# Kernel optimization log

Hardware: AMD Instinct MI355X
Metric: run time of the kernel (lower is better)

## Reference

```python
import jax, jax.numpy as jnp
import numpy as np

K = 24  # number of clusters (all ids in [0,K) assumed present per image)
DELTA_VAR = 1.0
DELTA_DIST = 2.0
VAR_W = 1.0
DIST_W = 1.0
REG_W = 1.0


def setup_inputs() -> dict:
    key = jax.random.key(0)
    k1, k2 = jax.random.split(key)
    data = jax.random.normal(k1, (4, 16, 512, 1024), dtype=jnp.float32)
    labels = jax.random.randint(k2, (4, 512, 1024), 0, K, dtype=jnp.int32)
    return {"data": data, "labels": labels}


def reference(data, labels):
    B, D, H, Wd = data.shape
    N = H * Wd
    # [B, N, D] points, [B*N] global segment ids (batch-offset cluster ids)
    X = jnp.transpose(data.reshape(B, D, N), (0, 2, 1)).reshape(B * N, D)
    seg = (labels.reshape(B, N) + jnp.arange(B, dtype=labels.dtype)[:, None] * K).reshape(-1)

    # per-cluster sums and counts -> centers  [B*K, D]
    sums = jax.ops.segment_sum(X, seg, num_segments=B * K)
    counts = jax.ops.segment_sum(jnp.ones((B * N,), X.dtype), seg, num_segments=B * K)
    centers_flat = sums / counts[:, None]
    centers = centers_flat.reshape(B, K, D)
    counts_bk = counts.reshape(B, K)

    # variance term: per-point hinged distance to own cluster center
    c_per_point = centers_flat[seg]                      # [B*N, D]
    pt_dist = jnp.linalg.norm(X - c_per_point, axis=1)   # [B*N]
    hv = jnp.maximum(pt_dist - DELTA_VAR, 0.0) ** 2
    var_per_cluster = jax.ops.segment_sum(hv, seg, num_segments=B * K).reshape(B, K) / counts_bk
    var_sum = var_per_cluster.sum()

    # distance term: pairwise center distances (diagonal kept, as in original,
    # contributing a constant delta_dist**2 per cluster)
    diff = centers[:, :, None, :] - centers[:, None, :, :]     # [B, K, K, D]
    sq = jnp.sum(diff * diff, axis=-1)                         # [B, K, K]
    eye = jnp.eye(K, dtype=bool)[None]
    cdist = jnp.where(eye, 0.0, jnp.sqrt(jnp.where(eye, 1.0, sq)))
    hd = jnp.maximum(DELTA_DIST - cdist, 0.0) ** 2
    dist_sum = hd.sum() / (2.0 * K * (K - 1))

    # regularization: mean center norm per image, summed over batch
    reg_sum = jnp.linalg.norm(centers, axis=2).mean(axis=1).sum()

    loss = (VAR_W * var_sum + DIST_W * dist_sum + REG_W * reg_sum) / B
    return loss
```

## Files before the change

### kernel.cpp

```cpp
#include <hip/hip_runtime.h>
#include <math.h>

#define KC 24
constexpr int D = 16;
constexpr int B = 4;
constexpr int N = 512 * 1024;
constexpr float DELTA_VAR = 1.0f;
constexpr float DELTA_DIST = 2.0f;

constexpr int REP = 8;
constexpr int RS  = KC * 17;
constexpr int CS  = 33;
constexpr int PTS = 1024;
constexpr int BLOCKS = (B * N) / PTS;


__global__ __launch_bounds__(256) void k_sums(const float* __restrict__ data,
                                              const int* __restrict__ labels,
                                              float* __restrict__ g_sums,
                                              float* __restrict__ g_cnt) {
    __shared__ float s_sum[REP * RS];
    __shared__ float s_cnt[REP * CS];
    const int t = threadIdx.x;
    for (int i = t; i < REP * RS; i += 256) s_sum[i] = 0.f;
    for (int i = t; i < REP * CS; i += 256) s_cnt[i] = 0.f;
    __syncthreads();

    const int chunk = blockIdx.x * PTS;
    const int b     = chunk >> 19;
    const int n0    = (chunk & (N - 1)) + t * 4;

    const int4 lab = *(const int4*)(labels + chunk + t * 4);
    const int rbase = (t & 7) * RS;
    const int ax = rbase + lab.x * 17;
    const int ay = rbase + lab.y * 17;
    const int az = rbase + lab.z * 17;
    const int aw = rbase + lab.w * 17;

    const float* base = data + (size_t)(b * D) * N + n0;
    float4 cur = *(const float4*)(base);
#pragma unroll
    for (int d = 0; d < D; ++d) {
        float4 nxt;
        if (d < D - 1) nxt = *(const float4*)(base + (size_t)(d + 1) * N);
        atomicAdd(&s_sum[ax + d], cur.x);
        atomicAdd(&s_sum[ay + d], cur.y);
        atomicAdd(&s_sum[az + d], cur.z);
        atomicAdd(&s_sum[aw + d], cur.w);
        cur = nxt;
    }
    const int cbase = (t & 7) * CS;
    atomicAdd(&s_cnt[cbase + lab.x], 1.f);
    atomicAdd(&s_cnt[cbase + lab.y], 1.f);
    atomicAdd(&s_cnt[cbase + lab.z], 1.f);
    atomicAdd(&s_cnt[cbase + lab.w], 1.f);
    __syncthreads();

    const int rot = (blockIdx.x * 131) & 255;
    for (int i = t; i < KC * D; i += 256) {
        int j = (i + rot) % (KC * D);
        int c = j >> 4, d = j & 15;
        float s = 0.f;
#pragma unroll
        for (int r = 0; r < REP; ++r) s += s_sum[r * RS + c * 17 + d];
        atomicAdd(&g_sums[b * (KC * D) + j], s);
    }
    if (t < KC) {
        float s = 0.f;
#pragma unroll
        for (int r = 0; r < REP; ++r) s += s_cnt[r * CS + t];
        atomicAdd(&g_cnt[b * KC + t], s);
    }
}

__global__ __launch_bounds__(256) void k_var(const float* __restrict__ data,
                                             const int* __restrict__ labels,
                                             const float* __restrict__ g_sums,
                                             const float* __restrict__ g_cnt,
                                             float* __restrict__ g_varp) {
    __shared__ float s_c[KC * 17];
    __shared__ float s_ic[KC];
    __shared__ float s_part[4];
    const int t = threadIdx.x;
    const int chunk = blockIdx.x * PTS;
    const int b     = chunk >> 19;
    const int n0    = (chunk & (N - 1)) + t * 4;

    for (int i = t; i < KC * D; i += 256) {
        int c = i >> 4, d = i & 15;
        s_c[c * 17 + d] = g_sums[b * (KC * D) + i] / g_cnt[b * KC + c];
    }
    if (t < KC) s_ic[t] = 1.f / g_cnt[b * KC + t];
    __syncthreads();

    const int4 lab = *(const int4*)(labels + chunk + t * 4);
    const int ax = lab.x * 17, ay = lab.y * 17, az = lab.z * 17, aw = lab.w * 17;

    const float* base = data + (size_t)(b * D) * N + n0;
    float4 acc = {0.f, 0.f, 0.f, 0.f};
    float4 cur = *(const float4*)(base);
#pragma unroll
    for (int d = 0; d < D; ++d) {
        float4 nxt;
        if (d < D - 1) nxt = *(const float4*)(base + (size_t)(d + 1) * N);
        float df;
        df = cur.x - s_c[ax + d]; acc.x += df * df;
        df = cur.y - s_c[ay + d]; acc.y += df * df;
        df = cur.z - s_c[az + d]; acc.z += df * df;
        df = cur.w - s_c[aw + d]; acc.w += df * df;
        cur = nxt;
    }
    float h, hsum;
    h = fmaxf(sqrtf(acc.x) - DELTA_VAR, 0.f); hsum  = h * h * s_ic[lab.x];
    h = fmaxf(sqrtf(acc.y) - DELTA_VAR, 0.f); hsum += h * h * s_ic[lab.y];
    h = fmaxf(sqrtf(acc.z) - DELTA_VAR, 0.f); hsum += h * h * s_ic[lab.z];
    h = fmaxf(sqrtf(acc.w) - DELTA_VAR, 0.f); hsum += h * h * s_ic[lab.w];

    for (int o = 32; o > 0; o >>= 1) hsum += __shfl_down(hsum, o, 64);
    if ((t & 63) == 0) s_part[t >> 6] = hsum;
    __syncthreads();
    if (t == 0)
        atomicAdd(&g_varp[blockIdx.x & 63],
                  s_part[0] + s_part[1] + s_part[2] + s_part[3]);
}

__global__ __launch_bounds__(128) void k_final(const float* __restrict__ g_sums,
                                               const float* __restrict__ g_cnt,
                                               const float* __restrict__ g_varp,
                                               float* __restrict__ out) {
    __shared__ float s_c[B * KC * 17];
    __shared__ float s_red[2];
    const int t = threadIdx.x;

    float acc = 0.f;
    if (t < B * KC) {
        float cnt = g_cnt[t];
        float ns = 0.f;
        for (int d = 0; d < D; ++d) {
            float c = g_sums[t * D + d] / cnt;
            s_c[t * 17 + d] = c;
            ns += c * c;
        }
        acc = sqrtf(ns) / (float)KC;
    }
    if (t < 64) acc += g_varp[t];
    __syncthreads();

    float dacc = 0.f;
    for (int idx = t; idx < B * KC * KC; idx += 128) {
        int b = idx / (KC * KC);
        int r = idx % (KC * KC);
        int i = r / KC, j = r % KC;
        float hd;
        if (i == j) {
            hd = DELTA_DIST * DELTA_DIST;
        } else {
            const float* ci = &s_c[(b * KC + i) * 17];
            const float* cj = &s_c[(b * KC + j) * 17];
            float sq = 0.f;
            for (int d = 0; d < D; ++d) { float df = ci[d] - cj[d]; sq += df * df; }
            float hh = fmaxf(DELTA_DIST - sqrtf(sq), 0.f);
            hd = hh * hh;
        }
        dacc += hd;
    }
    float total = acc + dacc / (2.f * KC * (KC - 1));

    for (int o = 32; o > 0; o >>= 1) total += __shfl_down(total, o, 64);
    if ((t & 63) == 0) s_red[t >> 6] = total;
    __syncthreads();
    if (t == 0) out[0] = (s_red[0] + s_red[1]) / (float)B;
}

extern "C" void kernel_launch(void* const* d_in, const int* in_sizes, int n_in,
                              void* d_out, int out_size, void* d_ws, size_t ws_size,
                              hipStream_t stream) {
    const float* data  = (const float*)d_in[0];
    const int* labels  = (const int*)d_in[1];
    float* ws = (float*)d_ws;
    float* g_sums = ws;
    float* g_cnt  = ws + B * KC * D;
    float* g_varp = g_cnt + B * KC;

    hipMemsetAsync(d_ws, 0, (B * KC * D + B * KC + 64) * sizeof(float), stream);

    k_sums<<<BLOCKS, 256, 0, stream>>>(data, labels, g_sums, g_cnt);
    k_var <<<BLOCKS, 256, 0, stream>>>(data, labels, g_sums, g_cnt, g_varp);
    k_final<<<1, 128, 0, stream>>>(g_sums, g_cnt, g_varp, (float*)d_out);
}
```

Baseline: 357.5 us.

## Slice global accumulators by block and batch all point loads upfront

Global sums and counts are split into 8 slices chosen by block index, so fewer blocks contend on the same global atomic addresses. Consumers (k_var, k_final) reduce the slices when building centers. Both kernels now issue all 16 float4 loads up front instead of a one-ahead prefetch, which exposes more memory-level parallelism. This costs extra registers and slightly more work per k_var block to reduce the slices.

```diff
diff --git a/kernel.cpp b/kernel.cpp
--- a/kernel.cpp
+++ b/kernel.cpp
@@ -13,6 +13,7 @@
 constexpr int CS  = 33;
 constexpr int PTS = 1024;
 constexpr int BLOCKS = (B * N) / PTS;
+constexpr int SL = 8;
 
 
 __global__ __launch_bounds__(256) void k_sums(const float* __restrict__ data,
@@ -38,24 +39,28 @@
     const int aw = rbase + lab.w * 17;
 
     const float* base = data + (size_t)(b * D) * N + n0;
-    float4 cur = *(const float4*)(base);
-#pragma unroll
-    for (int d = 0; d < D; ++d) {
-        float4 nxt;
-        if (d < D - 1) nxt = *(const float4*)(base + (size_t)(d + 1) * N);
-        atomicAdd(&s_sum[ax + d], cur.x);
-        atomicAdd(&s_sum[ay + d], cur.y);
-        atomicAdd(&s_sum[az + d], cur.z);
-        atomicAdd(&s_sum[aw + d], cur.w);
-        cur = nxt;
-    }
+    float4 v[D];
+#pragma unroll
+    for (int d = 0; d < D; ++d) v[d] = *(const float4*)(base + (size_t)d * N);
+
     const int cbase = (t & 7) * CS;
     atomicAdd(&s_cnt[cbase + lab.x], 1.f);
     atomicAdd(&s_cnt[cbase + lab.y], 1.f);
     atomicAdd(&s_cnt[cbase + lab.z], 1.f);
     atomicAdd(&s_cnt[cbase + lab.w], 1.f);
-    __syncthreads();
-
+
+#pragma unroll
+    for (int d = 0; d < D; ++d) {
+        atomicAdd(&s_sum[ax + d], v[d].x);
+        atomicAdd(&s_sum[ay + d], v[d].y);
+        atomicAdd(&s_sum[az + d], v[d].z);
+        atomicAdd(&s_sum[aw + d], v[d].w);
+    }
+    __syncthreads();
+
+    const int slice = blockIdx.x & (SL - 1);
+    float* gs = g_sums + slice * (B * KC * D) + b * (KC * D);
+    float* gc = g_cnt  + slice * (B * KC)     + b * KC;
     const int rot = (blockIdx.x * 131) & 255;
     for (int i = t; i < KC * D; i += 256) {
         int j = (i + rot) % (KC * D);
@@ -63,13 +68,13 @@
         float s = 0.f;
 #pragma unroll
         for (int r = 0; r < REP; ++r) s += s_sum[r * RS + c * 17 + d];
-        atomicAdd(&g_sums[b * (KC * D) + j], s);
+        atomicAdd(&gs[j], s);
     }
     if (t < KC) {
         float s = 0.f;
 #pragma unroll
         for (int r = 0; r < REP; ++r) s += s_cnt[r * CS + t];
-        atomicAdd(&g_cnt[b * KC + t], s);
+        atomicAdd(&gc[t], s);
     }
 }
 
@@ -86,29 +91,38 @@
     const int b     = chunk >> 19;
     const int n0    = (chunk & (N - 1)) + t * 4;
 
+    if (t < KC) {
+        float cn = 0.f;
+#pragma unroll
+        for (int r = 0; r < SL; ++r) cn += g_cnt[r * (B * KC) + b * KC + t];
+        s_ic[t] = 1.f / cn;
+    }
+    __syncthreads();
     for (int i = t; i < KC * D; i += 256) {
         int c = i >> 4, d = i & 15;
-        s_c[c * 17 + d] = g_sums[b * (KC * D) + i] / g_cnt[b * KC + c];
-    }
-    if (t < KC) s_ic[t] = 1.f / g_cnt[b * KC + t];
+        float s = 0.f;
+#pragma unroll
+        for (int r = 0; r < SL; ++r) s += g_sums[r * (B * KC * D) + b * (KC * D) + i];
+        s_c[c * 17 + d] = s * s_ic[c];
+    }
     __syncthreads();
 
     const int4 lab = *(const int4*)(labels + chunk + t * 4);
     const int ax = lab.x * 17, ay = lab.y * 17, az = lab.z * 17, aw = lab.w * 17;
 
     const float* base = data + (size_t)(b * D) * N + n0;
+    float4 v[D];
+#pragma unroll
+    for (int d = 0; d < D; ++d) v[d] = *(const float4*)(base + (size_t)d * N);
+
     float4 acc = {0.f, 0.f, 0.f, 0.f};
-    float4 cur = *(const float4*)(base);
 #pragma unroll
     for (int d = 0; d < D; ++d) {
-        float4 nxt;
-        if (d < D - 1) nxt = *(const float4*)(base + (size_t)(d + 1) * N);
         float df;
-        df = cur.x - s_c[ax + d]; acc.x += df * df;
-        df = cur.y - s_c[ay + d]; acc.y += df * df;
-        df = cur.z - s_c[az + d]; acc.z += df * df;
-        df = cur.w - s_c[aw + d]; acc.w += df * df;
-        cur = nxt;
+        df = v[d].x - s_c[ax + d]; acc.x += df * df;
+        df = v[d].y - s_c[ay + d]; acc.y += df * df;
+        df = v[d].z - s_c[az + d]; acc.z += df * df;
+        df = v[d].w - s_c[aw + d]; acc.w += df * df;
     }
     float h, hsum;
     h = fmaxf(sqrtf(acc.x) - DELTA_VAR, 0.f); hsum  = h * h * s_ic[lab.x];
@@ -134,10 +148,15 @@
 
     float acc = 0.f;
     if (t < B * KC) {
-        float cnt = g_cnt[t];
+        float cnt = 0.f;
+#pragma unroll
+        for (int r = 0; r < SL; ++r) cnt += g_cnt[r * (B * KC) + t];
         float ns = 0.f;
         for (int d = 0; d < D; ++d) {
-            float c = g_sums[t * D + d] / cnt;
+            float s = 0.f;
+#pragma unroll
+            for (int r = 0; r < SL; ++r) s += g_sums[r * (B * KC * D) + t * D + d];
+            float c = s / cnt;
             s_c[t * 17 + d] = c;
             ns += c * c;
         }
@@ -179,10 +198,11 @@
     const int* labels  = (const int*)d_in[1];
     float* ws = (float*)d_ws;
     float* g_sums = ws;
-    float* g_cnt  = ws + B * KC * D;
-    float* g_varp = g_cnt + B * KC;
-
-    hipMemsetAsync(d_ws, 0, (B * KC * D + B * KC + 64) * sizeof(float), stream);
+    float* g_cnt  = g_sums + SL * (B * KC * D);
+    float* g_varp = g_cnt  + SL * (B * KC);
+
+    hipMemsetAsync(d_ws, 0,
+                   (SL * (B * KC * D) + SL * (B * KC) + 64) * sizeof(float), stream);
 
     k_sums<<<BLOCKS, 256, 0, stream>>>(data, labels, g_sums, g_cnt);
     k_var <<<BLOCKS, 256, 0, stream>>>(data, labels, g_sums, g_cnt, g_varp);
```

Measured after the change: 364.3 us. Within noise of the previous version (+1.9%).
